# Optimization experiments

Measured on AMD Instinct MI355X. Metric: run time of the kernel, lower is better.

## Reference

```python
import jax, jax.numpy as jnp
import numpy as np

ORDER = 12      # Coef_num in the original
BLOCK = 1024
N_FFT = 2046    # torch.stft(n_fft=2046) -> 1024 onesided bins
HOP = 511       # torch default n_fft // 4
WORN = 1024
G1, G2 = 0.92, 0.6


def burg_lpc(y):
    """Burg's method LPC (exactly librosa.lpc), vectorized over blocks. y: [B, N] -> [B, ORDER+1]."""
    ar = jnp.zeros((y.shape[0], ORDER + 1), y.dtype).at[:, 0].set(1.0)
    f = y[:, 1:]
    b = y[:, :-1]
    den = jnp.sum(f * f, -1) + jnp.sum(b * b, -1)
    for i in range(ORDER):
        k = -2.0 * jnp.sum(b * f, -1) / den                     # reflection coeff [B]
        js = np.arange(1, i + 2)
        ar = ar.at[:, js].set(ar[:, js] + k[:, None] * ar[:, i - js + 1])
        f_new = f + k[:, None] * b
        b = b + k[:, None] * f
        f = f_new
        den = (1.0 - k * k) * den - b[:, -1] ** 2 - f[:, 0] ** 2
        f = f[:, 1:]
        b = b[:, :-1]
    return ar


def perceptual_weights(y):
    """Stacked |freqz| weight matrix [n_blocks*11, 1024], matching the original append order."""
    n_blocks = y.shape[0] // BLOCK
    yb = y[: n_blocks * BLOCK].reshape(n_blocks, BLOCK)
    lpc = burg_lpc(yb)[:, :ORDER]                               # original drops coeff index 12
    j = np.arange(ORDER)
    a1 = (lpc * (G1 ** j)).astype(jnp.complex64)                # denominator coeffs (bandwidth-expanded)
    a2 = (lpc * (G2 ** j)).astype(jnp.complex64)                # numerator coeffs
    omega = jnp.pi * jnp.arange(WORN) / WORN                    # freqz worN=1024 digital freqs
    E = jnp.exp(-1j * omega[:, None] * j[None, :]).astype(jnp.complex64)   # [F, 12]
    # freqz is called inside the k1 loop: at step k1 only coeffs 0..k1 are filled -> triangular mask
    M = jnp.asarray(j[None, :] <= np.arange(1, ORDER)[:, None], jnp.complex64)  # [11, 12]
    num = jnp.einsum('bj,kj,fj->bkf', a2, M, E)
    den = jnp.einsum('bj,kj,fj->bkf', a1, M, E)
    return jnp.abs(num / den).reshape(n_blocks * (ORDER - 1), WORN)


def stft_mag(x):
    """torch.stft(x, n_fft=2046, center=True, reflect pad, rect window, onesided) magnitude -> [1024, n_frames]."""
    pad = N_FFT // 2
    xp = jnp.pad(x, (pad, pad), mode='reflect')
    n_frames = 1 + x.shape[0] // HOP
    idx = jnp.arange(n_frames)[:, None] * HOP + jnp.arange(N_FFT)[None, :]
    frames = xp[idx]                                            # [n_frames, 2046]
    return jnp.abs(jnp.fft.rfft(frames, axis=1)).T              # [1024, n_frames]


def setup_inputs() -> dict:
    key = jax.random.key(0)
    kx, ky = jax.random.split(key)
    L = 2048 * 1024
    x = jax.random.normal(kx, (L,), dtype=jnp.float32)
    y = jax.random.normal(ky, (L,), dtype=jnp.float32)
    return {"x": x, "y": y}


def reference(x, y):
    W = jax.lax.stop_gradient(perceptual_weights(y))            # original computes weights on detached numpy
    Sx = stft_mag(x)
    Sy = stft_mag(y)
    mse = jnp.mean((Sx - Sy) ** 2, axis=1)                      # [1024] per-frequency-bin MSE over frames
    return jnp.mean(mse[None, :] / W)                           # broadcast over [n_blocks*11, 1024]
```

## Files before the change

### kernel.cpp

```cpp
#include <hip/hip_runtime.h>
#include <hip/hip_bf16.h>
#include <hip/hip_fp8.h>

#define PI_D 3.14159265358979323846
#define L_TOTAL 2097152
#define NFRAMES 4105
#define NBLK    4108
#define MROWS_P 8216
#define MPAD    8320
#define KP      512
#define NDIM    2048
#define PSTRIDE 8224

#define COMBINE_BLOCKS 4352
#define INVW_BLOCKS 512


#define BURG_BLOCKS   512
#define FRAMES_BLOCKS 1040
#define BASIS_BLOCKS  256
#define SARR_BLOCKS   17
#define PREP_BLOCKS   (BURG_BLOCKS + FRAMES_BLOCKS + BASIS_BLOCKS + SARR_BLOCKS)

typedef __attribute__((ext_vector_type(8))) short short8;
typedef __attribute__((ext_vector_type(4))) short short4v;
typedef __attribute__((ext_vector_type(4))) float floatx4;
typedef float floatx4u __attribute__((ext_vector_type(4), aligned(4)));

typedef __attribute__((address_space(1))) void gvoid_as1;
typedef __attribute__((address_space(3))) void lvoid_as3;

__device__ __forceinline__ void gld_lds16(const void* g, void* l) {
    __builtin_amdgcn_global_load_lds((gvoid_as1*)g, (lvoid_as3*)l, 16, 0, 0);
}

__device__ __forceinline__ float b2f(short v) {
    unsigned int u = ((unsigned int)(unsigned short)v) << 16;
    return __uint_as_float(u);
}

__device__ __forceinline__ unsigned int pk4_e4m3(float a, float b, float c, float d) {
    __hip_fp8_e4m3 q0(a), q1(b), q2(c), q3(d);
    return (unsigned int)q0.__x | ((unsigned int)q1.__x << 8)
         | ((unsigned int)q2.__x << 16) | ((unsigned int)q3.__x << 24);
}

__device__ __forceinline__ float xorall(float v) {
    v += __shfl_xor(v, 1, 64);
    v += __shfl_xor(v, 2, 64);
    v += __shfl_xor(v, 4, 64);
    v += __shfl_xor(v, 8, 64);
    v += __shfl_xor(v, 16, 64);
    v += __shfl_xor(v, 32, 64);
    return v;
}

__device__ __forceinline__ float wave_reduce(float v) {
    v += __shfl_down(v, 32, 64);
    v += __shfl_down(v, 16, 64);
    v += __shfl_down(v, 8, 64);
    v += __shfl_down(v, 4, 64);
    v += __shfl_down(v, 2, 64);
    v += __shfl_down(v, 1, 64);
    return v;
}

__device__ __forceinline__ void frames_body(int bid, int tid,
                                            const float* __restrict__ x,
                                            const float* __restrict__ y,
                                            char* __restrict__ A) {
    const int lane = tid & 63;
    const int b = bid * 4 + (tid >> 6);
    const int p0 = b * 511 + lane * 8 - 1023;
    float xv[8], yv[8];
    if (p0 >= 0 && p0 + 8 <= L_TOTAL) {
        floatx4u x0 = *(const floatx4u*)(x + p0);
        floatx4u x1 = *(const floatx4u*)(x + p0 + 4);
        floatx4u y0 = *(const floatx4u*)(y + p0);
        floatx4u y1 = *(const floatx4u*)(y + p0 + 4);
#pragma unroll
        for (int e = 0; e < 4; e++) { xv[e] = x0[e]; xv[4 + e] = x1[e]; }
#pragma unroll
        for (int e = 0; e < 4; e++) { yv[e] = y0[e]; yv[4 + e] = y1[e]; }
    } else {
#pragma unroll
        for (int e = 0; e < 8; e++) {
            int p = p0 + e;
            if (p < 0) p = -p;
            else if (p >= L_TOTAL) p = 2 * L_TOTAL - 2 - p;
            xv[e] = x[p];
            yv[e] = y[p];
        }
    }
    int4 pk;
    pk.x = (int)pk4_e4m3(xv[0], xv[1], xv[2], xv[3]);
    pk.y = (int)pk4_e4m3(xv[4], xv[5], xv[6], xv[7]);
    pk.z = (int)pk4_e4m3(yv[0], yv[1], yv[2], yv[3]);
    pk.w = (int)pk4_e4m3(yv[4], yv[5], yv[6], yv[7]);
    *(int4*)(A + (size_t)(b >> 3) * 8192 + lane * 128 + (b & 7) * 16) = pk;
}

__device__ __forceinline__ void basis_body(int bid, int tid,
                                           char* __restrict__ Bt) {
    const int lane = tid & 63;
    const int f = bid * 4 + (tid >> 6);
    const int n0 = lane * 8;
    const int m0 = (f * n0) % 2046;
    float s, c, ss, cs;
    __sincosf((float)m0 * (float)(PI_D / 1023.0), &s, &c);
    __sincosf((float)f * (float)(PI_D / 1023.0), &ss, &cs);
    float cv[8], sv[8];
#pragma unroll
    for (int e = 0; e < 8; e++) {
        const int n = n0 + e;
        const bool valid = n < 511;
        cv[e] = valid ? c : 0.f;
        sv[e] = valid ? -s : 0.f;
        float c2 = c * cs - s * ss;
        float s2 = s * cs + c * ss;
        c = c2; s = s2;
    }
    int4 pk;
    pk.x = (int)pk4_e4m3(cv[0], cv[1], cv[2], cv[3]);
    pk.y = (int)pk4_e4m3(cv[4], cv[5], cv[6], cv[7]);
    pk.z = (int)pk4_e4m3(sv[0], sv[1], sv[2], sv[3]);
    pk.w = (int)pk4_e4m3(sv[4], sv[5], sv[6], sv[7]);
    *(int4*)(Bt + (size_t)(f >> 3) * 8192 + lane * 128 + (f & 7) * 16) = pk;
}

__device__ __forceinline__ void sarr_body(int bid, int tid,
                                          const float* __restrict__ x,
                                          const float* __restrict__ y,
                                          float4* __restrict__ S,
                                          float* __restrict__ wsf) {
    if (bid < 8) wsf[bid * 256 + tid] = 0.f;
    const int b = bid * 256 + tid;
    int p0 = 511 * b - 1023;
    int p1 = p0 + 1;
    int m0 = (p0 < 0) ? -p0 : ((p0 >= L_TOTAL) ? 2 * L_TOTAL - 2 - p0 : p0);
    int m1 = (p1 < 0) ? -p1 : ((p1 >= L_TOTAL) ? 2 * L_TOTAL - 2 - p1 : p1);
    S[b] = make_float4(x[m0], x[m1], y[m0], y[m1]);
}

__device__ __forceinline__ void burg_body(int bid, int tid,
                                          const float* __restrict__ y,
                                          float* __restrict__ ar_out) {
    const int lane = tid & 63;
    const int wid = tid >> 6;
    const int blk = bid * 4 + wid;
    const float4* yb4 = (const float4*)(y + (size_t)blk * 1024) + lane * 4;

    float t[16];
#pragma unroll
    for (int q = 0; q < 4; q++) {
        float4 v = yb4[q];
        t[q * 4 + 0] = v.x; t[q * 4 + 1] = v.y;
        t[q * 4 + 2] = v.z; t[q * 4 + 3] = v.w;
    }
    float b[16], f[16];
#pragma unroll
    for (int r = 0; r < 16; r++) b[r] = t[r];
#pragma unroll
    for (int r = 0; r < 15; r++) f[r] = t[r + 1];
    {
        float nb = __shfl_down(t[0], 1, 64);
        f[15] = (lane == 63) ? 0.f : nb;
        if (lane == 63) b[15] = 0.f;
    }

    float den = 0.f;
#pragma unroll
    for (int r = 0; r < 16; r++) den += f[r] * f[r] + b[r] * b[r];
    den = xorall(den);

    float ar_s[13];
    ar_s[0] = 1.f;
#pragma unroll
    for (int j = 1; j < 13; j++) ar_s[j] = 0.f;

#pragma unroll
    for (int i = 0; i < 12; i++) {
        float num = 0.f;
#pragma unroll
        for (int r = 0; r < 16; r++) num += f[r] * b[r];
        num = xorall(num);
        const float k = -2.f * num / den;

        float fu[16], bu[16];
#pragma unroll
        for (int r = 0; r < 16; r++) {
            fu[r] = f[r] + k * b[r];
            bu[r] = b[r] + k * f[r];
        }
        const float f0 = __shfl(fu[0], 0, 64);
        const int pos = 1022 - i;
        const int L = pos >> 4, S = pos & 15;
        const float blast = __shfl(bu[S], L, 64);

        den = (1.f - k * k) * den - blast * blast - f0 * f0;

        float nf = __shfl_down(fu[0], 1, 64);
#pragma unroll
        for (int r = 0; r < 15; r++) f[r] = fu[r + 1];
        f[15] = (lane == 63) ? 0.f : nf;
#pragma unroll
        for (int r = 0; r < 16; r++) b[r] = bu[r];
        if (lane == L) b[S] = 0.f;

        float tmp[13];
#pragma unroll
        for (int js = 1; js <= i + 1; js++) tmp[js] = ar_s[js] + k * ar_s[i + 1 - js];
#pragma unroll
        for (int js = 1; js <= i + 1; js++) ar_s[js] = tmp[js];
    }

#pragma unroll
    for (int j = 0; j < 12; j++)
        if (lane == j) ar_out[(size_t)blk * 12 + j] = ar_s[j];
}

__global__ __launch_bounds__(256) void prep_kernel(const float* __restrict__ x,
                                                   const float* __restrict__ y,
                                                   char* __restrict__ A,
                                                   char* __restrict__ Bt,
                                                   float4* __restrict__ S,
                                                   float* __restrict__ ar,
                                                   float* __restrict__ wsf) {
    const int bid = blockIdx.x;
    const int tid = threadIdx.x;
    if (bid < BURG_BLOCKS) {
        burg_body(bid, tid, y, ar);
    } else if (bid < BURG_BLOCKS + FRAMES_BLOCKS) {
        frames_body(bid - BURG_BLOCKS, tid, x, y, A);
    } else if (bid < BURG_BLOCKS + FRAMES_BLOCKS + BASIS_BLOCKS) {
        basis_body(bid - BURG_BLOCKS - FRAMES_BLOCKS, tid, Bt);
    } else {
        sarr_body(bid - BURG_BLOCKS - FRAMES_BLOCKS - BASIS_BLOCKS, tid, x, y, S, wsf);
    }
}

__global__ __launch_bounds__(512, 4) void gemm_p_kernel(
    const char* __restrict__ A, const char* __restrict__ Bt,
    __hip_bfloat16* __restrict__ Pt) {
    __shared__ __align__(16) char smem[8192];

    const int tid = threadIdx.x;
    const int lane = tid & 63;
    const int w = tid >> 6;
    const int wm = w >> 1;
    const int wn = w & 1;
    const int q = lane >> 4, l15 = lane & 15;
    const int tileN = blockIdx.x * 128;
    const int tileM = blockIdx.y * 128;

    floatx4 acc[2][4];
#pragma unroll
    for (int i = 0; i < 2; i++)
#pragma unroll
        for (int j = 0; j < 4; j++) acc[i][j] = (floatx4){0.f, 0.f, 0.f, 0.f};

    const int t8 = tid & 255;
    const int g = t8 >> 5;
    const int u = t8 & 31;
    const char* p = ((tid < 256)
        ? A + (((size_t)(tileM >> 4) + g) << 13)
        : Bt + (((size_t)(tileN >> 4) + g) << 13)) + u * 16;

    for (int it = 0; it < KP / 32; it++) {
        gld_lds16(p, smem + tid * 16);
        p += 512;
        __syncthreads();

        long af[2], bf[4];
#pragma unroll
        for (int sm = 0; sm < 2; sm++)
            af[sm] = *(const long*)(smem + (wm * 2 + sm) * 512 + lane * 8);
#pragma unroll
        for (int sn = 0; sn < 4; sn++)
            bf[sn] = *(const long*)(smem + 4096 + (wn * 4 + sn) * 512 + lane * 8);
#pragma unroll
        for (int sm = 0; sm < 2; sm++)
#pragma unroll
            for (int sn = 0; sn < 4; sn++)
                acc[sm][sn] = __builtin_amdgcn_mfma_f32_16x16x32_fp8_fp8(
                    af[sm], bf[sn], acc[sm][sn], 0, 0, 0);
        __syncthreads();
    }

#pragma unroll
    for (int sm = 0; sm < 2; sm++) {
        const int rowBase = tileM + wm * 32 + sm * 16 + q * 4;
        if (rowBase >= MROWS_P) continue;
#pragma unroll
        for (int sn = 0; sn < 4; sn++) {
            const int colG = tileN + wn * 64 + sn * 16 + l15;
            short4v pk;
#pragma unroll
            for (int r = 0; r < 4; r++) {
                __hip_bfloat16 h = __float2bfloat16(acc[sm][sn][r]);
                pk[r] = *(short*)&h;
            }
            *(short4v*)((char*)Pt + ((size_t)colG * PSTRIDE + rowBase) * 2) = pk;
        }
    }
}

__device__ __forceinline__ void combine_body(int bx, int ty, int tid,
                                             const __hip_bfloat16* __restrict__ Pt,
                                             const float4* __restrict__ S,
                                             float* __restrict__ mse_sum) {
    const int lane = tid & 63;
    const int wid = tid >> 6;
    const int f = bx * 4 + wid;

    float wc[4], ws[4];
    wc[0] = 1.f; ws[0] = 0.f;
#pragma unroll
    for (int h = 1; h < 4; h++) {
        int m = (511 * h * f) % 2046;
        float s, c;
        __sincosf((float)m * (float)(PI_D / 1023.0), &s, &c);
        wc[h] = c; ws[h] = -s;
    }
    float wtc0, wts0, wtc1, wts1;
    {
        int m = (2044 * f) % 2046;
        float s, c;
        __sincosf((float)m * (float)(PI_D / 1023.0), &s, &c);
        wtc0 = c; wts0 = -s;
        m = (2045 * f) % 2046;
        __sincosf((float)m * (float)(PI_D / 1023.0), &s, &c);
        wtc1 = c; wts1 = -s;
    }

    const __hip_bfloat16* rowRe = Pt + (size_t)(2 * f) * PSTRIDE;
    const __hip_bfloat16* rowIm = rowRe + PSTRIDE;

    float acc = 0.f;
    const int tt0 = ty * 256 + 4 * lane;
    if (tt0 < NFRAMES) {
        short8 re0 = *(const short8*)(rowRe + 2 * tt0);
        short8 re1 = *(const short8*)(rowRe + 2 * tt0 + 8);
        short8 im0 = *(const short8*)(rowIm + 2 * tt0);
        short8 im1 = *(const short8*)(rowIm + 2 * tt0 + 8);
        float4 sT[4];
#pragma unroll
        for (int d = 0; d < 4; d++) sT[d] = S[tt0 + 4 + d];
        float vr[16], vi[16];
#pragma unroll
        for (int j = 0; j < 8; j++) {
            vr[j] = b2f(re0[j]); vr[j + 8] = b2f(re1[j]);
            vi[j] = b2f(im0[j]); vi[j + 8] = b2f(im1[j]);
        }
#pragma unroll
        for (int d = 0; d < 4; d++) {
            const int tt = tt0 + d;
            if (tt >= NFRAMES) break;
            float xr = 0.f, xi = 0.f, yr = 0.f, yi = 0.f;
#pragma unroll
            for (int h = 0; h < 4; h++) {
                const int qx = 2 * d + 2 * h;
                xr += wc[h] * vr[qx] - ws[h] * vi[qx];
                xi += wc[h] * vi[qx] + ws[h] * vr[qx];
                const int qy = qx + 1;
                yr += wc[h] * vr[qy] - ws[h] * vi[qy];
                yi += wc[h] * vi[qy] + ws[h] * vr[qy];
            }
            const float4 sd = sT[d];
            xr += wtc0 * sd.x + wtc1 * sd.y;
            xi += wts0 * sd.x + wts1 * sd.y;
            yr += wtc0 * sd.z + wtc1 * sd.w;
            yi += wts0 * sd.z + wts1 * sd.w;
            float dm = sqrtf(xr * xr + xi * xi) - sqrtf(yr * yr + yi * yi);
            acc += dm * dm;
        }
    }
    acc = xorall(acc);
    if (lane == 0) atomicAdd(&mse_sum[f], acc);
}

__device__ __forceinline__ void invw_body(int bid, int tid,
                                          const float* __restrict__ ar,
                                          float* __restrict__ invW) {
    __shared__ float sar[16][12];
    const int f = (bid & 3) * 256 + tid;
    const int b0 = (bid >> 2) * 16;
    if (tid < 16 * 12) ((float*)sar)[tid] = ar[(size_t)b0 * 12 + tid];
    __syncthreads();

    const float omega = (float)(PI_D / 1024.0) * (float)f;
    float sw, cw;
    __sincosf(omega, &sw, &cw);

    float acc = 0.f;
#pragma unroll 4
    for (int bb = 0; bb < 16; bb++) {
        float a0 = sar[bb][0];
        float nr = a0, ni = 0.f, dr = a0, di = 0.f;
        float er = 1.f, ei = 0.f;
        float g1p = 1.f, g2p = 1.f;
#pragma unroll
        for (int j = 1; j < 12; j++) {
            float er2 = er * cw + ei * sw;
            float ei2 = ei * cw - er * sw;
            er = er2; ei = ei2;
            g1p *= 0.92f; g2p *= 0.6f;
            float aj = sar[bb][j];
            float a1 = aj * g1p, a2 = aj * g2p;
            nr += a2 * er; ni += a2 * ei;
            dr += a1 * er; di += a1 * ei;
            float D = dr * dr + di * di;
            float Nn = nr * nr + ni * ni;
            acc += D * __builtin_amdgcn_rsqf(D * Nn);
        }
    }
    atomicAdd(&invW[f], acc);
}

__global__ __launch_bounds__(256) void combine_invw_kernel(
    const __hip_bfloat16* __restrict__ Pt,
    const float4* __restrict__ S,
    float* __restrict__ mse_sum,
    const float* __restrict__ ar,
    float* __restrict__ invW) {
    const int bid = blockIdx.x;
    const int tid = threadIdx.x;
    if (bid < INVW_BLOCKS) {
        invw_body(bid, tid, ar, invW);
    } else {
        const int cb = bid - INVW_BLOCKS;
        combine_body(cb & 255, cb >> 8, tid, Pt, S, mse_sum);
    }
}

__global__ void final_kernel(const float* __restrict__ mse_sum,
                             const float* __restrict__ invW,
                             float* __restrict__ out) {
    __shared__ float red[4];
    const int tid = threadIdx.x;
    float lo = 0.f;
    for (int f = tid; f < 1024; f += 256) lo += mse_sum[f] * invW[f];
    lo = wave_reduce(lo);
    if ((tid & 63) == 0) red[tid >> 6] = lo;
    __syncthreads();
    if (tid == 0) {
        float tot = red[0] + red[1] + red[2] + red[3];
        out[0] = tot * (float)(1.0 / (4105.0 * 22528.0 * 1024.0));
    }
}

extern "C" void kernel_launch(void* const* d_in, const int* in_sizes, int n_in,
                              void* d_out, int out_size, void* d_ws, size_t ws_size,
                              hipStream_t stream) {
    const float* x = (const float*)d_in[0];
    const float* y = (const float*)d_in[1];
    float* out = (float*)d_out;

    float* wsf = (float*)d_ws;
    float* mse_sum = wsf;
    float* invW = wsf + 1024;
    float* ar = wsf + 2080;
    float4* S = (float4*)((char*)d_ws + 131072);
    char* Ap = (char*)d_ws + 262144;
    char* Bp = (char*)d_ws + 4521984;
    __hip_bfloat16* Pt = (__hip_bfloat16*)((char*)d_ws + 8388608);

    prep_kernel<<<PREP_BLOCKS, 256, 0, stream>>>(x, y, Ap, Bp, S, ar, wsf);
    gemm_p_kernel<<<dim3(NDIM / 128, MPAD / 128), 512, 0, stream>>>(Ap, Bp, Pt);
    combine_invw_kernel<<<INVW_BLOCKS + COMBINE_BLOCKS, 256, 0, stream>>>(Pt, S, mse_sum, ar, invW);
    final_kernel<<<1, 256, 0, stream>>>(mse_sum, invW, out);
}
```

Before: 125.4 us.

## Fuse FP8 GEMM with STFT combine epilogue and invW into one kernel

The separate GEMM kernel that wrote a bf16 P matrix to global memory is merged with the combine step. Each tile now keeps its bf16 results in LDS and immediately forms the per-frame spectra and squared magnitude differences, reducing them per bin before one atomic per bin. The M tiling changes to 56-frame overlapping blocks (74 tiles) so the 4-block hop overlap is available inside a tile. The invW work is folded into the same launch with 512-thread blocks. This removes the Pt global write and read and one kernel launch, at the cost of recomputing overlapping GEMM rows, higher LDS use per block and lower occupancy.

```diff
diff --git a/kernel.cpp b/kernel.cpp
--- a/kernel.cpp
+++ b/kernel.cpp
@@ -7,14 +7,14 @@
 #define NFRAMES 4105
 #define NBLK    4108
 #define MROWS_P 8216
-#define MPAD    8320
 #define KP      512
 #define NDIM    2048
-#define PSTRIDE 8224
-
-#define COMBINE_BLOCKS 4352
-#define INVW_BLOCKS 512
-
+
+
+#define MTILES 74
+#define NTILES 16
+#define INVW_BLOCKS 256
+#define GC_BLOCKS (MTILES * NTILES)
 
 #define BURG_BLOCKS   512
 #define FRAMES_BLOCKS 1040
@@ -23,7 +23,6 @@
 #define PREP_BLOCKS   (BURG_BLOCKS + FRAMES_BLOCKS + BASIS_BLOCKS + SARR_BLOCKS)
 
 typedef __attribute__((ext_vector_type(8))) short short8;
-typedef __attribute__((ext_vector_type(4))) short short4v;
 typedef __attribute__((ext_vector_type(4))) float floatx4;
 typedef float floatx4u __attribute__((ext_vector_type(4), aligned(4)));
 
@@ -32,11 +31,6 @@
 
 __device__ __forceinline__ void gld_lds16(const void* g, void* l) {
     __builtin_amdgcn_global_load_lds((gvoid_as1*)g, (lvoid_as3*)l, 16, 0, 0);
-}
-
-__device__ __forceinline__ float b2f(short v) {
-    unsigned int u = ((unsigned int)(unsigned short)v) << 16;
-    return __uint_as_float(u);
 }
 
 __device__ __forceinline__ unsigned int pk4_e4m3(float a, float b, float c, float d) {
@@ -239,152 +233,12 @@
     }
 }
 
-__global__ __launch_bounds__(512, 4) void gemm_p_kernel(
-    const char* __restrict__ A, const char* __restrict__ Bt,
-    __hip_bfloat16* __restrict__ Pt) {
-    __shared__ __align__(16) char smem[8192];
-
-    const int tid = threadIdx.x;
-    const int lane = tid & 63;
-    const int w = tid >> 6;
-    const int wm = w >> 1;
-    const int wn = w & 1;
-    const int q = lane >> 4, l15 = lane & 15;
-    const int tileN = blockIdx.x * 128;
-    const int tileM = blockIdx.y * 128;
-
-    floatx4 acc[2][4];
-#pragma unroll
-    for (int i = 0; i < 2; i++)
-#pragma unroll
-        for (int j = 0; j < 4; j++) acc[i][j] = (floatx4){0.f, 0.f, 0.f, 0.f};
-
-    const int t8 = tid & 255;
-    const int g = t8 >> 5;
-    const int u = t8 & 31;
-    const char* p = ((tid < 256)
-        ? A + (((size_t)(tileM >> 4) + g) << 13)
-        : Bt + (((size_t)(tileN >> 4) + g) << 13)) + u * 16;
-
-    for (int it = 0; it < KP / 32; it++) {
-        gld_lds16(p, smem + tid * 16);
-        p += 512;
-        __syncthreads();
-
-        long af[2], bf[4];
-#pragma unroll
-        for (int sm = 0; sm < 2; sm++)
-            af[sm] = *(const long*)(smem + (wm * 2 + sm) * 512 + lane * 8);
-#pragma unroll
-        for (int sn = 0; sn < 4; sn++)
-            bf[sn] = *(const long*)(smem + 4096 + (wn * 4 + sn) * 512 + lane * 8);
-#pragma unroll
-        for (int sm = 0; sm < 2; sm++)
-#pragma unroll
-            for (int sn = 0; sn < 4; sn++)
-                acc[sm][sn] = __builtin_amdgcn_mfma_f32_16x16x32_fp8_fp8(
-                    af[sm], bf[sn], acc[sm][sn], 0, 0, 0);
-        __syncthreads();
-    }
-
-#pragma unroll
-    for (int sm = 0; sm < 2; sm++) {
-        const int rowBase = tileM + wm * 32 + sm * 16 + q * 4;
-        if (rowBase >= MROWS_P) continue;
-#pragma unroll
-        for (int sn = 0; sn < 4; sn++) {
-            const int colG = tileN + wn * 64 + sn * 16 + l15;
-            short4v pk;
-#pragma unroll
-            for (int r = 0; r < 4; r++) {
-                __hip_bfloat16 h = __float2bfloat16(acc[sm][sn][r]);
-                pk[r] = *(short*)&h;
-            }
-            *(short4v*)((char*)Pt + ((size_t)colG * PSTRIDE + rowBase) * 2) = pk;
-        }
-    }
-}
-
-__device__ __forceinline__ void combine_body(int bx, int ty, int tid,
-                                             const __hip_bfloat16* __restrict__ Pt,
-                                             const float4* __restrict__ S,
-                                             float* __restrict__ mse_sum) {
-    const int lane = tid & 63;
-    const int wid = tid >> 6;
-    const int f = bx * 4 + wid;
-
-    float wc[4], ws[4];
-    wc[0] = 1.f; ws[0] = 0.f;
-#pragma unroll
-    for (int h = 1; h < 4; h++) {
-        int m = (511 * h * f) % 2046;
-        float s, c;
-        __sincosf((float)m * (float)(PI_D / 1023.0), &s, &c);
-        wc[h] = c; ws[h] = -s;
-    }
-    float wtc0, wts0, wtc1, wts1;
-    {
-        int m = (2044 * f) % 2046;
-        float s, c;
-        __sincosf((float)m * (float)(PI_D / 1023.0), &s, &c);
-        wtc0 = c; wts0 = -s;
-        m = (2045 * f) % 2046;
-        __sincosf((float)m * (float)(PI_D / 1023.0), &s, &c);
-        wtc1 = c; wts1 = -s;
-    }
-
-    const __hip_bfloat16* rowRe = Pt + (size_t)(2 * f) * PSTRIDE;
-    const __hip_bfloat16* rowIm = rowRe + PSTRIDE;
-
-    float acc = 0.f;
-    const int tt0 = ty * 256 + 4 * lane;
-    if (tt0 < NFRAMES) {
-        short8 re0 = *(const short8*)(rowRe + 2 * tt0);
-        short8 re1 = *(const short8*)(rowRe + 2 * tt0 + 8);
-        short8 im0 = *(const short8*)(rowIm + 2 * tt0);
-        short8 im1 = *(const short8*)(rowIm + 2 * tt0 + 8);
-        float4 sT[4];
-#pragma unroll
-        for (int d = 0; d < 4; d++) sT[d] = S[tt0 + 4 + d];
-        float vr[16], vi[16];
-#pragma unroll
-        for (int j = 0; j < 8; j++) {
-            vr[j] = b2f(re0[j]); vr[j + 8] = b2f(re1[j]);
-            vi[j] = b2f(im0[j]); vi[j + 8] = b2f(im1[j]);
-        }
-#pragma unroll
-        for (int d = 0; d < 4; d++) {
-            const int tt = tt0 + d;
-            if (tt >= NFRAMES) break;
-            float xr = 0.f, xi = 0.f, yr = 0.f, yi = 0.f;
-#pragma unroll
-            for (int h = 0; h < 4; h++) {
-                const int qx = 2 * d + 2 * h;
-                xr += wc[h] * vr[qx] - ws[h] * vi[qx];
-                xi += wc[h] * vi[qx] + ws[h] * vr[qx];
-                const int qy = qx + 1;
-                yr += wc[h] * vr[qy] - ws[h] * vi[qy];
-                yi += wc[h] * vi[qy] + ws[h] * vr[qy];
-            }
-            const float4 sd = sT[d];
-            xr += wtc0 * sd.x + wtc1 * sd.y;
-            xi += wts0 * sd.x + wts1 * sd.y;
-            yr += wtc0 * sd.z + wtc1 * sd.w;
-            yi += wts0 * sd.z + wts1 * sd.w;
-            float dm = sqrtf(xr * xr + xi * xi) - sqrtf(yr * yr + yi * yi);
-            acc += dm * dm;
-        }
-    }
-    acc = xorall(acc);
-    if (lane == 0) atomicAdd(&mse_sum[f], acc);
-}
-
-__device__ __forceinline__ void invw_body(int bid, int tid,
+__device__ __forceinline__ void invw_body(int bid, int tid, char* smem,
                                           const float* __restrict__ ar,
                                           float* __restrict__ invW) {
-    __shared__ float sar[16][12];
-    const int f = (bid & 3) * 256 + tid;
-    const int b0 = (bid >> 2) * 16;
+    float (*sar)[12] = (float(*)[12])smem;
+    const int f = (bid & 1) * 512 + tid;
+    const int b0 = (bid >> 1) * 16;
     if (tid < 16 * 12) ((float*)sar)[tid] = ar[(size_t)b0 * 12 + tid];
     __syncthreads();
 
@@ -417,19 +271,142 @@
     atomicAdd(&invW[f], acc);
 }
 
-__global__ __launch_bounds__(256) void combine_invw_kernel(
-    const __hip_bfloat16* __restrict__ Pt,
-    const float4* __restrict__ S,
-    float* __restrict__ mse_sum,
-    const float* __restrict__ ar,
-    float* __restrict__ invW) {
+__device__ __forceinline__ void gemm_combine_body(
+    int bx, int by, int tid, char* smem,
+    const char* __restrict__ A, const char* __restrict__ Bt,
+    const float4* __restrict__ S, float* __restrict__ mse_sum) {
+    char* stg = smem;
+    unsigned short* Cl = (unsigned short*)(smem + 8192);
+    float* msePart = (float*)(smem + 8192 + 32768);
+
+    const int tid9 = tid;
+    const int lane = tid9 & 63;
+    const int w = tid9 >> 6;
+    const int wm = w >> 1, wn = w & 1;
+    const int q = lane >> 4, l15 = lane & 15;
+    const int tileN = bx * 128;
+    const int tileMblk = by * 56;
+    const int tileM = tileMblk * 2;
+
+    if (tid9 < 64) msePart[tid9] = 0.f;
+
+    floatx4 acc[2][4];
+#pragma unroll
+    for (int i = 0; i < 2; i++)
+#pragma unroll
+        for (int j = 0; j < 4; j++) acc[i][j] = (floatx4){0.f, 0.f, 0.f, 0.f};
+
+    const int t8 = tid9 & 255;
+    const int g = t8 >> 5;
+    const int u = t8 & 31;
+    const char* p = ((tid9 < 256)
+        ? A + (((size_t)(tileM >> 4) + g) << 13)
+        : Bt + (((size_t)(tileN >> 4) + g) << 13)) + u * 16;
+
+    for (int it = 0; it < KP / 32; it++) {
+        gld_lds16(p, stg + tid9 * 16);
+        p += 512;
+        __syncthreads();
+
+        long af[2], bf[4];
+#pragma unroll
+        for (int sm = 0; sm < 2; sm++)
+            af[sm] = *(const long*)(stg + (wm * 2 + sm) * 512 + lane * 8);
+#pragma unroll
+        for (int sn = 0; sn < 4; sn++)
+            bf[sn] = *(const long*)(stg + 4096 + (wn * 4 + sn) * 512 + lane * 8);
+#pragma unroll
+        for (int sm = 0; sm < 2; sm++)
+#pragma unroll
+            for (int sn = 0; sn < 4; sn++)
+                acc[sm][sn] = __builtin_amdgcn_mfma_f32_16x16x32_fp8_fp8(
+                    af[sm], bf[sn], acc[sm][sn], 0, 0, 0);
+        __syncthreads();
+    }
+
+#pragma unroll
+    for (int sm = 0; sm < 2; sm++) {
+        const int rowB = wm * 32 + sm * 16 + q * 4;
+#pragma unroll
+        for (int sn = 0; sn < 4; sn++) {
+            const int col = wn * 64 + sn * 16 + l15;
+#pragma unroll
+            for (int r = 0; r < 4; r++) {
+                __hip_bfloat16 h = __float2bfloat16(acc[sm][sn][r]);
+                Cl[(rowB + r) * 128 + col] = *(unsigned short*)&h;
+            }
+        }
+    }
+    __syncthreads();
+
+    const int fg = (tileN >> 1) + lane;
+    float wc[4], ws[4];
+    wc[0] = 1.f; ws[0] = 0.f;
+#pragma unroll
+    for (int h = 1; h < 4; h++) {
+        int m = (511 * h * fg) % 2046;
+        float s, c;
+        __sincosf((float)m * (float)(PI_D / 1023.0), &s, &c);
+        wc[h] = c; ws[h] = -s;
+    }
+    float wtc0, wts0, wtc1, wts1;
+    {
+        int m = (2044 * fg) % 2046;
+        float s, c;
+        __sincosf((float)m * (float)(PI_D / 1023.0), &s, &c);
+        wtc0 = c; wts0 = -s;
+        m = (2045 * fg) % 2046;
+        __sincosf((float)m * (float)(PI_D / 1023.0), &s, &c);
+        wtc1 = c; wts1 = -s;
+    }
+
+    const unsigned int* Cd = (const unsigned int*)Cl;
+    float accm = 0.f;
+#pragma unroll
+    for (int d = 0; d < 7; d++) {
+        const int tl = w * 7 + d;
+        const int tg = tileMblk + tl;
+        if (tg >= NFRAMES) break;
+        float xr = 0.f, xi = 0.f, yr = 0.f, yi = 0.f;
+#pragma unroll
+        for (int h = 0; h < 4; h++) {
+            const int bl = tl + h;
+            unsigned int ux = Cd[(2 * bl) * 64 + lane];
+            unsigned int uy = Cd[(2 * bl + 1) * 64 + lane];
+            float vrx = __uint_as_float(ux << 16);
+            float vix = __uint_as_float(ux & 0xFFFF0000u);
+            float vry = __uint_as_float(uy << 16);
+            float viy = __uint_as_float(uy & 0xFFFF0000u);
+            xr += wc[h] * vrx - ws[h] * vix;
+            xi += wc[h] * vix + ws[h] * vrx;
+            yr += wc[h] * vry - ws[h] * viy;
+            yi += wc[h] * viy + ws[h] * vry;
+        }
+        const float4 sd = S[tg + 4];
+        xr += wtc0 * sd.x + wtc1 * sd.y;
+        xi += wts0 * sd.x + wts1 * sd.y;
+        yr += wtc0 * sd.z + wtc1 * sd.w;
+        yi += wts0 * sd.z + wts1 * sd.w;
+        float dm = sqrtf(xr * xr + xi * xi) - sqrtf(yr * yr + yi * yi);
+        accm += dm * dm;
+    }
+    atomicAdd(&msePart[lane], accm);
+    __syncthreads();
+    if (tid9 < 64) atomicAdd(&mse_sum[(tileN >> 1) + tid9], msePart[tid9]);
+}
+
+__global__ __launch_bounds__(512, 4) void gemm_combine_kernel(
+    const char* __restrict__ A, const char* __restrict__ Bt,
+    const float4* __restrict__ S, float* __restrict__ mse_sum,
+    const float* __restrict__ ar, float* __restrict__ invW) {
+    __shared__ __align__(16) char smem[8192 + 32768 + 256];
     const int bid = blockIdx.x;
     const int tid = threadIdx.x;
     if (bid < INVW_BLOCKS) {
-        invw_body(bid, tid, ar, invW);
+        invw_body(bid, tid, smem, ar, invW);
     } else {
-        const int cb = bid - INVW_BLOCKS;
-        combine_body(cb & 255, cb >> 8, tid, Pt, S, mse_sum);
+        const int b = bid - INVW_BLOCKS;
+        gemm_combine_body(b & 15, b >> 4, tid, smem, A, Bt, S, mse_sum);
     }
 }
 
@@ -463,10 +440,8 @@
     float4* S = (float4*)((char*)d_ws + 131072);
     char* Ap = (char*)d_ws + 262144;
     char* Bp = (char*)d_ws + 4521984;
-    __hip_bfloat16* Pt = (__hip_bfloat16*)((char*)d_ws + 8388608);
 
     prep_kernel<<<PREP_BLOCKS, 256, 0, stream>>>(x, y, Ap, Bp, S, ar, wsf);
-    gemm_p_kernel<<<dim3(NDIM / 128, MPAD / 128), 512, 0, stream>>>(Ap, Bp, Pt);
-    combine_invw_kernel<<<INVW_BLOCKS + COMBINE_BLOCKS, 256, 0, stream>>>(Pt, S, mse_sum, ar, invW);
+    gemm_combine_kernel<<<INVW_BLOCKS + GC_BLOCKS, 512, 0, stream>>>(Ap, Bp, S, mse_sum, ar, invW);
     final_kernel<<<1, 256, 0, stream>>>(mse_sum, invW, out);
 }
```

Result: faster. 119.2 us (-4.9%).
